# Kernel optimization log

Hardware: AMD Instinct MI355X
Metric: run time of the kernel (lower is better)

## Reference

```python
import jax, jax.numpy as jnp
import numpy as np

N = 200000
M = 100000
K = 27
C = 128
NEG_SLOPE = 0.2


def setup_inputs() -> dict:
    key = jax.random.key(0)
    ks = jax.random.split(key, 7)
    feats = jax.random.normal(ks[0], (N, C), dtype=jnp.float32)
    # small init scale (mirrors xavier * 0.1) to keep activations stable through 27-tap convs
    W1 = jax.random.normal(ks[1], (K, C, C), dtype=jnp.float32) * 0.02
    W2 = jax.random.normal(ks[2], (C, C), dtype=jnp.float32) * 0.05
    W3 = jax.random.normal(ks[3], (K, C, C), dtype=jnp.float32) * 0.02
    in_map = jax.random.randint(ks[4], (K, M), 0, N, dtype=jnp.int32)
    out_map = jax.random.randint(ks[5], (K, M), 0, N, dtype=jnp.int32)
    mask = jax.random.uniform(ks[6], (N, 1), dtype=jnp.float32)
    return {"feats": feats, "W1": W1, "W2": W2, "W3": W3,
            "in_map": in_map, "out_map": out_map, "mask": mask}


def _lrelu(x):
    return jnp.where(x >= 0, x, NEG_SLOPE * x)


def _sparse_conv(feats, W, in_map, out_map, n_out):
    """Gather-GEMM-scatter sparse conv: scan over K kernel offsets.

    feats: [N, Cin]; W: [K, Cin, Cout]; in_map/out_map: [K, M].
    """
    def body(acc, xs):
        im, om, w = xs
        y = feats[im] @ w                    # [M, Cin] @ [Cin, Cout]
        return acc.at[om].add(y), None
    out0 = jnp.zeros((n_out, W.shape[-1]), feats.dtype)
    out, _ = jax.lax.scan(body, out0, (in_map, out_map, W))
    return out


def reference(feats, W1, W2, W3, in_map, out_map, mask):
    n = feats.shape[0]
    c1 = _lrelu(_sparse_conv(feats, W1, in_map, out_map, n))   # conv1 (k=3) + LeakyReLU
    c2 = _lrelu(c1 @ W2)                                       # conv2 (k=1) + LeakyReLU
    c3 = _sparse_conv(c2, W3, in_map, out_map, n)              # conv3 (k=3)
    return c3 * mask
```

## Files before the change

kernel.cpp:

```cpp
#include <hip/hip_runtime.h>
#include <hip/hip_bf16.h>


typedef __attribute__((ext_vector_type(8))) short short8;
typedef __attribute__((ext_vector_type(4))) float f32x4;

#define CDIM 128
#define BM   128
#define NEG_SLOPE 0.2f

__device__ __forceinline__ unsigned short f2bf(float x) {
    union { float f; unsigned u; } un; un.f = x;
    unsigned r = un.u + 0x7fffu + ((un.u >> 16) & 1u);
    return (unsigned short)(r >> 16);
}

__device__ __forceinline__ float lrelu(float x) {
    return x >= 0.f ? x : NEG_SLOPE * x;
}

__device__ __forceinline__ int swz(int r, int c) {
    return (r << 7) + ((((c >> 3) ^ (r & 15)) << 3));
}

__global__ void cvt_feats_kernel(const float* __restrict__ in,
                                 unsigned short* __restrict__ out, int n4) {
    int i = blockIdx.x * blockDim.x + threadIdx.x;
    if (i >= n4) return;
    float4 v = reinterpret_cast<const float4*>(in)[i];
    ushort4 o;
    o.x = f2bf(v.x); o.y = f2bf(v.y); o.z = f2bf(v.z); o.w = f2bf(v.w);
    reinterpret_cast<ushort4*>(out)[i] = o;
}

__global__ void cvt_weights_kernel(const float* __restrict__ W1,
                                   const float* __restrict__ W2,
                                   const float* __restrict__ W3,
                                   unsigned short* __restrict__ W1t,
                                   unsigned short* __restrict__ W2t,
                                   unsigned short* __restrict__ W3t) {
    const int KW = 27 * 128 * 128;
    int t = blockIdx.x * blockDim.x + threadIdx.x;
    if (t < KW) {
        int k = t >> 14, r = t & 16383, n = r >> 7, kk = r & 127;
        W1t[t] = f2bf(W1[(k << 14) + (kk << 7) + n]);
    } else if (t < 2 * KW) {
        int t2 = t - KW;
        int k = t2 >> 14, r = t2 & 16383, n = r >> 7, kk = r & 127;
        W3t[t2] = f2bf(W3[(k << 14) + (kk << 7) + n]);
    } else if (t < 2 * KW + 16384) {
        int t2 = t - 2 * KW;
        int n = t2 >> 7, kk = t2 & 127;
        W2t[t2] = f2bf(W2[(kk << 7) + n]);
    }
}

__global__ __launch_bounds__(256, 2)
void sconv_kernel(const unsigned short* __restrict__ A,
                  const unsigned short* __restrict__ Wt,
                  const int* __restrict__ in_map,
                  const int* __restrict__ out_map,
                  float* __restrict__ out,
                  int M) {
    const int k     = blockIdx.y;
    const int mbase = blockIdx.x * BM;
    const int tid   = threadIdx.x;

    __shared__ unsigned short lA[BM * CDIM];
    __shared__ unsigned short lW[CDIM * CDIM];

    const unsigned short* wk = Wt + (size_t)k * 16384;
    #pragma unroll
    for (int i = 0; i < 8; ++i) {
        int flat = (i * 256 + tid) * 8;
        int row = flat >> 7, col = flat & 127;
        short8 v = *reinterpret_cast<const short8*>(wk + flat);
        *reinterpret_cast<short8*>(&lW[swz(row, col)]) = v;
    }

    const int* imk = in_map + (size_t)k * M;
    #pragma unroll
    for (int p = 0; p < 8; ++p) {
        int r = p * 16 + (tid >> 4);
        int c = (tid & 15) * 8;
        int m = mbase + r;
        short8 v = {0, 0, 0, 0, 0, 0, 0, 0};
        if (m < M) {
            int arow = __ldg(imk + m);
            v = *reinterpret_cast<const short8*>(A + (size_t)arow * CDIM + c);
        }
        *reinterpret_cast<short8*>(&lA[swz(r, c)]) = v;
    }
    __syncthreads();

    const int wid  = tid >> 6, lane = tid & 63;
    const int wr   = (wid >> 1) * 64, wc = (wid & 1) * 64;
    const int lrow = lane & 15, quad = lane >> 4;

    f32x4 acc[4][4];
    #pragma unroll
    for (int i = 0; i < 4; ++i)
        #pragma unroll
        for (int j = 0; j < 4; ++j)
            acc[i][j] = {0.f, 0.f, 0.f, 0.f};

    #pragma unroll
    for (int s = 0; s < 4; ++s) {
        const int kf = s * 32 + quad * 8;
        short8 a[4], b[4];
        #pragma unroll
        for (int i = 0; i < 4; ++i)
            a[i] = *reinterpret_cast<const short8*>(&lA[swz(wr + i * 16 + lrow, kf)]);
        #pragma unroll
        for (int j = 0; j < 4; ++j)
            b[j] = *reinterpret_cast<const short8*>(&lW[swz(wc + j * 16 + lrow, kf)]);
        #pragma unroll
        for (int i = 0; i < 4; ++i)
            #pragma unroll
            for (int j = 0; j < 4; ++j)
                acc[i][j] = __builtin_amdgcn_mfma_f32_16x16x32_bf16(a[i], b[j], acc[i][j], 0, 0, 0);
    }

    const int* omk = out_map + (size_t)k * M;
    #pragma unroll
    for (int i = 0; i < 4; ++i) {
        #pragma unroll
        for (int reg = 0; reg < 4; ++reg) {
            int m = mbase + wr + i * 16 + quad * 4 + reg;
            if (m < M) {
                int orow = __ldg(omk + m);
                float* dst = out + (size_t)orow * CDIM + wc + lrow;
                #pragma unroll
                for (int j = 0; j < 4; ++j)
                    unsafeAtomicAdd(dst + j * 16, acc[i][j][reg]);
            }
        }
    }
}

__global__ __launch_bounds__(256, 2)
void conv2_kernel(const float* __restrict__ c1,
                  const unsigned short* __restrict__ W2t,
                  unsigned short* __restrict__ c2,
                  int M) {
    const int mbase = blockIdx.x * BM;
    const int tid   = threadIdx.x;

    __shared__ unsigned short lA[BM * CDIM];
    __shared__ unsigned short lW[CDIM * CDIM];

    #pragma unroll
    for (int i = 0; i < 8; ++i) {
        int flat = (i * 256 + tid) * 8;
        int row = flat >> 7, col = flat & 127;
        short8 v = *reinterpret_cast<const short8*>(W2t + flat);
        *reinterpret_cast<short8*>(&lW[swz(row, col)]) = v;
    }

    #pragma unroll
    for (int p = 0; p < 8; ++p) {
        int r = p * 16 + (tid >> 4);
        int c = (tid & 15) * 8;
        int m = mbase + r;
        unsigned short vv[8];
        if (m < M) {
            const float4* src = reinterpret_cast<const float4*>(c1 + (size_t)m * CDIM + c);
            float4 x0 = src[0], x1 = src[1];
            vv[0] = f2bf(lrelu(x0.x)); vv[1] = f2bf(lrelu(x0.y));
            vv[2] = f2bf(lrelu(x0.z)); vv[3] = f2bf(lrelu(x0.w));
            vv[4] = f2bf(lrelu(x1.x)); vv[5] = f2bf(lrelu(x1.y));
            vv[6] = f2bf(lrelu(x1.z)); vv[7] = f2bf(lrelu(x1.w));
        } else {
            #pragma unroll
            for (int q = 0; q < 8; ++q) vv[q] = 0;
        }
        short8 v;
        #pragma unroll
        for (int q = 0; q < 8; ++q) v[q] = (short)vv[q];
        *reinterpret_cast<short8*>(&lA[swz(r, c)]) = v;
    }
    __syncthreads();

    const int wid  = tid >> 6, lane = tid & 63;
    const int wr   = (wid >> 1) * 64, wc = (wid & 1) * 64;
    const int lrow = lane & 15, quad = lane >> 4;

    f32x4 acc[4][4];
    #pragma unroll
    for (int i = 0; i < 4; ++i)
        #pragma unroll
        for (int j = 0; j < 4; ++j)
            acc[i][j] = {0.f, 0.f, 0.f, 0.f};

    #pragma unroll
    for (int s = 0; s < 4; ++s) {
        const int kf = s * 32 + quad * 8;
        short8 a[4], b[4];
        #pragma unroll
        for (int i = 0; i < 4; ++i)
            a[i] = *reinterpret_cast<const short8*>(&lA[swz(wr + i * 16 + lrow, kf)]);
        #pragma unroll
        for (int j = 0; j < 4; ++j)
            b[j] = *reinterpret_cast<const short8*>(&lW[swz(wc + j * 16 + lrow, kf)]);
        #pragma unroll
        for (int i = 0; i < 4; ++i)
            #pragma unroll
            for (int j = 0; j < 4; ++j)
                acc[i][j] = __builtin_amdgcn_mfma_f32_16x16x32_bf16(a[i], b[j], acc[i][j], 0, 0, 0);
    }

    #pragma unroll
    for (int i = 0; i < 4; ++i) {
        #pragma unroll
        for (int reg = 0; reg < 4; ++reg) {
            int m = mbase + wr + i * 16 + quad * 4 + reg;
            if (m < M) {
                unsigned short* dst = c2 + (size_t)m * CDIM + wc + lrow;
                #pragma unroll
                for (int j = 0; j < 4; ++j)
                    dst[j * 16] = f2bf(lrelu(acc[i][j][reg]));
            }
        }
    }
}

__global__ void mask_mul_kernel(float* __restrict__ out,
                                const float* __restrict__ mask, int n4) {
    int i = blockIdx.x * blockDim.x + threadIdx.x;
    if (i >= n4) return;
    int row = i >> 5;
    float m = mask[row];
    float4 v = reinterpret_cast<float4*>(out)[i];
    v.x *= m; v.y *= m; v.z *= m; v.w *= m;
    reinterpret_cast<float4*>(out)[i] = v;
}

extern "C" void kernel_launch(void* const* d_in, const int* in_sizes, int n_in,
                              void* d_out, int out_size, void* d_ws, size_t ws_size,
                              hipStream_t stream) {
    const float* feats   = (const float*)d_in[0];
    const float* W1      = (const float*)d_in[1];
    const float* W2      = (const float*)d_in[2];
    const float* W3      = (const float*)d_in[3];
    const int*   in_map  = (const int*)d_in[4];
    const int*   out_map = (const int*)d_in[5];
    const float* mask    = (const float*)d_in[6];
    float*       out     = (float*)d_out;

    const int K = 27;
    const int N = in_sizes[0] / CDIM;
    const int M = in_sizes[4] / K;

    unsigned short* feats_bf = (unsigned short*)d_ws;
    unsigned short* c2_bf    = feats_bf + (size_t)N * CDIM;
    unsigned short* W1t      = c2_bf + (size_t)N * CDIM;
    unsigned short* W3t      = W1t + (size_t)K * CDIM * CDIM;
    unsigned short* W2t      = W3t + (size_t)K * CDIM * CDIM;
    size_t need = ((size_t)2 * N * CDIM + (size_t)2 * K * CDIM * CDIM + CDIM * CDIM) * 2;
    if (ws_size < need) return;

    const int n4 = N * CDIM / 4;
    cvt_feats_kernel<<<(n4 + 255) / 256, 256, 0, stream>>>(feats, feats_bf, n4);
    const int wtot = 2 * K * CDIM * CDIM + CDIM * CDIM;
    cvt_weights_kernel<<<(wtot + 255) / 256, 256, 0, stream>>>(W1, W2, W3, W1t, W2t, W3t);

    hipMemsetAsync(d_out, 0, (size_t)N * CDIM * sizeof(float), stream);

    dim3 gs((M + BM - 1) / BM, K);
    sconv_kernel<<<gs, 256, 0, stream>>>(feats_bf, W1t, in_map, out_map, out, M);

    conv2_kernel<<<(N + BM - 1) / BM, 256, 0, stream>>>(out, W2t, c2_bf, N);

    hipMemsetAsync(d_out, 0, (size_t)N * CDIM * sizeof(float), stream);
    sconv_kernel<<<gs, 256, 0, stream>>>(c2_bf, W3t, in_map, out_map, out, M);

    mask_mul_kernel<<<(n4 + 255) / 256, 256, 0, stream>>>(out, mask, n4);
}
```

Baseline: 2.530 ms.

## Bucket gather-scatter pairs by output tile and accumulate in LDS

Builds a per-output-tile, per-tap bucketing of (in_row, out_row, k) pairs with a histogram, a three-kernel scan and an atomic scatter. Each conv then runs one block per 128-row output tile, accumulating MFMA results into an LDS float tile with shared atomics instead of global atomics. LeakyReLU and bf16 conversion are fused into the conv1 epilogue and the mask multiply into the conv3 epilogue, which removes both output memsets and the standalone mask kernel. The cost is extra preprocessing kernels, weights read straight from global memory for every pair, and load imbalance because the grid is only about 1563 blocks.

```diff
diff --git a/kernel.cpp b/kernel.cpp
--- a/kernel.cpp
+++ b/kernel.cpp
@@ -7,6 +7,7 @@
 
 #define CDIM 128
 #define BM   128
+#define KTAPS 27
 #define NEG_SLOPE 0.2f
 
 __device__ __forceinline__ unsigned short f2bf(float x) {
@@ -39,7 +40,7 @@
                                    unsigned short* __restrict__ W1t,
                                    unsigned short* __restrict__ W2t,
                                    unsigned short* __restrict__ W3t) {
-    const int KW = 27 * 128 * 128;
+    const int KW = KTAPS * 128 * 128;
     int t = blockIdx.x * blockDim.x + threadIdx.x;
     if (t < KW) {
         int k = t >> 14, r = t & 16383, n = r >> 7, kk = r & 127;
@@ -55,40 +56,179 @@
     }
 }
 
+__global__ void hist_kernel(const int* __restrict__ out_map,
+                            int* __restrict__ cnt, int M) {
+    int m = blockIdx.x * 256 + threadIdx.x;
+    if (m >= M) return;
+    int k = blockIdx.y;
+    int orow = out_map[(size_t)k * M + m];
+    atomicAdd(cnt + ((orow >> 7) * KTAPS + k), 1);
+}
+
+__global__ void scan_a_kernel(const int* __restrict__ cnt, int* __restrict__ cs,
+                              int* __restrict__ partials, int NB) {
+    __shared__ int sd[256];
+    int tid = threadIdx.x, bin = blockIdx.x * 256 + tid;
+    int v = (bin < NB) ? ((cnt[bin] + 15) >> 4) : 0;
+    sd[tid] = v; __syncthreads();
+    for (int off = 1; off < 256; off <<= 1) {
+        int t = (tid >= off) ? sd[tid - off] : 0; __syncthreads();
+        sd[tid] += t; __syncthreads();
+    }
+    if (bin < NB) cs[bin] = sd[tid] - v;
+    if (tid == 255) partials[blockIdx.x] = sd[255];
+}
+
+__global__ void scan_b_kernel(int* __restrict__ partials, int NBb) {
+    __shared__ int sd[256];
+    int tid = threadIdx.x;
+    int v = (tid < NBb) ? partials[tid] : 0;
+    sd[tid] = v; __syncthreads();
+    for (int off = 1; off < 256; off <<= 1) {
+        int t = (tid >= off) ? sd[tid - off] : 0; __syncthreads();
+        sd[tid] += t; __syncthreads();
+    }
+    partials[tid] = sd[tid] - v;
+}
+
+__global__ void scan_c_kernel(int* __restrict__ cs, const int* __restrict__ partials,
+                              int NB, int NBb) {
+    int bin = blockIdx.x * 256 + threadIdx.x;
+    if (bin < NB) cs[bin] += partials[blockIdx.x];
+    if (bin == 0) cs[NB] = partials[NBb];
+}
+
+__global__ void fill_kernel(int* __restrict__ p, int n, int v) {
+    int i = blockIdx.x * 256 + threadIdx.x;
+    if (i < n) p[i] = v;
+}
+
+__global__ void scatter_kernel(const int* __restrict__ in_map,
+                               const int* __restrict__ out_map,
+                               const int* __restrict__ cs,
+                               int* __restrict__ cursor,
+                               int* __restrict__ pairs, int M) {
+    int m = blockIdx.x * 256 + threadIdx.x;
+    if (m >= M) return;
+    int k = blockIdx.y;
+    size_t e = (size_t)k * M + m;
+    int orow = out_map[e], irow = in_map[e];
+    int bin = (orow >> 7) * KTAPS + k;
+    int pos = atomicAdd(cursor + bin, 1);
+    pairs[(size_t)cs[bin] * 16 + pos] = (k << 26) | (irow << 8) | (orow & 127);
+}
+
+template<int MODE>
+__global__ __launch_bounds__(512, 4)
+void conv_fused_kernel(const unsigned short* __restrict__ A,
+                       const unsigned short* __restrict__ Wt,
+                       const int* __restrict__ pairs,
+                       const int* __restrict__ cs,
+                       unsigned short* __restrict__ bf_out,
+                       float* __restrict__ f_out,
+                       const float* __restrict__ mask,
+                       int N) {
+    __shared__ float lacc[128 * 128];
+    const int tid  = threadIdx.x;
+    const int tile = blockIdx.x;
+
+    #pragma unroll
+    for (int i = tid; i < 128 * 128 / 4; i += 512)
+        reinterpret_cast<f32x4*>(lacc)[i] = (f32x4){0.f, 0.f, 0.f, 0.f};
+    __syncthreads();
+
+    const int lo = cs[tile * KTAPS], hi = cs[tile * KTAPS + KTAPS];
+    const int wid = tid >> 6, lane = tid & 63;
+    const int lrow = lane & 15, quad = lane >> 4;
+
+    const int total = hi - lo;
+    const int per   = (total + 7) >> 3;
+    const int c0 = lo + wid * per;
+    const int c1 = (c0 + per < hi) ? (c0 + per) : hi;
+
+    for (int c = c0; c < c1; ++c) {
+        int pk   = pairs[c * 16 + lrow];
+        int irow = (pk >> 8) & 0x3FFFF;
+        int srow = pk & 0x7F;
+        int k    = ((unsigned)__shfl(pk, 0)) >> 26;
+
+        const unsigned short* wk = Wt + ((size_t)k << 14);
+        const unsigned short* ar = A + (size_t)irow * CDIM + quad * 8;
+        short8 a0 = *reinterpret_cast<const short8*>(ar);
+        short8 a1 = *reinterpret_cast<const short8*>(ar + 32);
+        short8 a2 = *reinterpret_cast<const short8*>(ar + 64);
+        short8 a3 = *reinterpret_cast<const short8*>(ar + 96);
+
+        int sr0 = __shfl(srow, quad * 4 + 0);
+        int sr1 = __shfl(srow, quad * 4 + 1);
+        int sr2 = __shfl(srow, quad * 4 + 2);
+        int sr3 = __shfl(srow, quad * 4 + 3);
+
+        #pragma unroll 2
+        for (int j = 0; j < 8; ++j) {
+            const unsigned short* wb = wk + ((j * 16 + lrow) << 7) + quad * 8;
+            f32x4 acc = {0.f, 0.f, 0.f, 0.f};
+            acc = __builtin_amdgcn_mfma_f32_16x16x32_bf16(a0, *reinterpret_cast<const short8*>(wb),      acc, 0, 0, 0);
+            acc = __builtin_amdgcn_mfma_f32_16x16x32_bf16(a1, *reinterpret_cast<const short8*>(wb + 32), acc, 0, 0, 0);
+            acc = __builtin_amdgcn_mfma_f32_16x16x32_bf16(a2, *reinterpret_cast<const short8*>(wb + 64), acc, 0, 0, 0);
+            acc = __builtin_amdgcn_mfma_f32_16x16x32_bf16(a3, *reinterpret_cast<const short8*>(wb + 96), acc, 0, 0, 0);
+            float* colp = lacc + j * 16 + lrow;
+            atomicAdd(colp + (sr0 << 7), acc[0]);
+            atomicAdd(colp + (sr1 << 7), acc[1]);
+            atomicAdd(colp + (sr2 << 7), acc[2]);
+            atomicAdd(colp + (sr3 << 7), acc[3]);
+        }
+    }
+    __syncthreads();
+
+    const int gbase = tile << 7;
+    #pragma unroll
+    for (int it = 0; it < 8; ++it) {
+        int flat = it * 512 + tid;
+        int r = flat >> 5, c4 = flat & 31;
+        int g = gbase + r;
+        if (g < N) {
+            f32x4 v = *reinterpret_cast<f32x4*>(&lacc[r * CDIM + c4 * 4]);
+            if (MODE == 0) {
+                ushort4 o;
+                o.x = f2bf(lrelu(v[0])); o.y = f2bf(lrelu(v[1]));
+                o.z = f2bf(lrelu(v[2])); o.w = f2bf(lrelu(v[3]));
+                *reinterpret_cast<ushort4*>(bf_out + (size_t)g * CDIM + c4 * 4) = o;
+            } else {
+                float mv = mask[g];
+                f32x4 o = {v[0] * mv, v[1] * mv, v[2] * mv, v[3] * mv};
+                *reinterpret_cast<f32x4*>(f_out + (size_t)g * CDIM + c4 * 4) = o;
+            }
+        }
+    }
+}
+
 __global__ __launch_bounds__(256, 2)
-void sconv_kernel(const unsigned short* __restrict__ A,
-                  const unsigned short* __restrict__ Wt,
-                  const int* __restrict__ in_map,
-                  const int* __restrict__ out_map,
-                  float* __restrict__ out,
-                  int M) {
-    const int k     = blockIdx.y;
+void conv2_kernel(const unsigned short* __restrict__ c1,
+                  const unsigned short* __restrict__ W2t,
+                  unsigned short* __restrict__ c2,
+                  int N) {
     const int mbase = blockIdx.x * BM;
     const int tid   = threadIdx.x;
 
     __shared__ unsigned short lA[BM * CDIM];
     __shared__ unsigned short lW[CDIM * CDIM];
 
-    const unsigned short* wk = Wt + (size_t)k * 16384;
     #pragma unroll
     for (int i = 0; i < 8; ++i) {
         int flat = (i * 256 + tid) * 8;
         int row = flat >> 7, col = flat & 127;
-        short8 v = *reinterpret_cast<const short8*>(wk + flat);
+        short8 v = *reinterpret_cast<const short8*>(W2t + flat);
         *reinterpret_cast<short8*>(&lW[swz(row, col)]) = v;
     }
 
-    const int* imk = in_map + (size_t)k * M;
     #pragma unroll
     for (int p = 0; p < 8; ++p) {
         int r = p * 16 + (tid >> 4);
         int c = (tid & 15) * 8;
         int m = mbase + r;
         short8 v = {0, 0, 0, 0, 0, 0, 0, 0};
-        if (m < M) {
-            int arow = __ldg(imk + m);
-            v = *reinterpret_cast<const short8*>(A + (size_t)arow * CDIM + c);
-        }
+        if (m < N) v = *reinterpret_cast<const short8*>(c1 + (size_t)m * CDIM + c);
         *reinterpret_cast<short8*>(&lA[swz(r, c)]) = v;
     }
     __syncthreads();
@@ -121,100 +261,12 @@
                 acc[i][j] = __builtin_amdgcn_mfma_f32_16x16x32_bf16(a[i], b[j], acc[i][j], 0, 0, 0);
     }
 
-    const int* omk = out_map + (size_t)k * M;
     #pragma unroll
     for (int i = 0; i < 4; ++i) {
         #pragma unroll
         for (int reg = 0; reg < 4; ++reg) {
             int m = mbase + wr + i * 16 + quad * 4 + reg;
-            if (m < M) {
-                int orow = __ldg(omk + m);
-                float* dst = out + (size_t)orow * CDIM + wc + lrow;
-                #pragma unroll
-                for (int j = 0; j < 4; ++j)
-                    unsafeAtomicAdd(dst + j * 16, acc[i][j][reg]);
-            }
-        }
-    }
-}
-
-__global__ __launch_bounds__(256, 2)
-void conv2_kernel(const float* __restrict__ c1,
-                  const unsigned short* __restrict__ W2t,
-                  unsigned short* __restrict__ c2,
-                  int M) {
-    const int mbase = blockIdx.x * BM;
-    const int tid   = threadIdx.x;
-
-    __shared__ unsigned short lA[BM * CDIM];
-    __shared__ unsigned short lW[CDIM * CDIM];
-
-    #pragma unroll
-    for (int i = 0; i < 8; ++i) {
-        int flat = (i * 256 + tid) * 8;
-        int row = flat >> 7, col = flat & 127;
-        short8 v = *reinterpret_cast<const short8*>(W2t + flat);
-        *reinterpret_cast<short8*>(&lW[swz(row, col)]) = v;
-    }
-
-    #pragma unroll
-    for (int p = 0; p < 8; ++p) {
-        int r = p * 16 + (tid >> 4);
-        int c = (tid & 15) * 8;
-        int m = mbase + r;
-        unsigned short vv[8];
-        if (m < M) {
-            const float4* src = reinterpret_cast<const float4*>(c1 + (size_t)m * CDIM + c);
-            float4 x0 = src[0], x1 = src[1];
-            vv[0] = f2bf(lrelu(x0.x)); vv[1] = f2bf(lrelu(x0.y));
-            vv[2] = f2bf(lrelu(x0.z)); vv[3] = f2bf(lrelu(x0.w));
-            vv[4] = f2bf(lrelu(x1.x)); vv[5] = f2bf(lrelu(x1.y));
-            vv[6] = f2bf(lrelu(x1.z)); vv[7] = f2bf(lrelu(x1.w));
-        } else {
-            #pragma unroll
-            for (int q = 0; q < 8; ++q) vv[q] = 0;
-        }
-        short8 v;
-        #pragma unroll
-        for (int q = 0; q < 8; ++q) v[q] = (short)vv[q];
-        *reinterpret_cast<short8*>(&lA[swz(r, c)]) = v;
-    }
-    __syncthreads();
-
-    const int wid  = tid >> 6, lane = tid & 63;
-    const int wr   = (wid >> 1) * 64, wc = (wid & 1) * 64;
-    const int lrow = lane & 15, quad = lane >> 4;
-
-    f32x4 acc[4][4];
-    #pragma unroll
-    for (int i = 0; i < 4; ++i)
-        #pragma unroll
-        for (int j = 0; j < 4; ++j)
-            acc[i][j] = {0.f, 0.f, 0.f, 0.f};
-
-    #pragma unroll
-    for (int s = 0; s < 4; ++s) {
-        const int kf = s * 32 + quad * 8;
-        short8 a[4], b[4];
-        #pragma unroll
-        for (int i = 0; i < 4; ++i)
-            a[i] = *reinterpret_cast<const short8*>(&lA[swz(wr + i * 16 + lrow, kf)]);
-        #pragma unroll
-        for (int j = 0; j < 4; ++j)
-            b[j] = *reinterpret_cast<const short8*>(&lW[swz(wc + j * 16 + lrow, kf)]);
-        #pragma unroll
-        for (int i = 0; i < 4; ++i)
-            #pragma unroll
-            for (int j = 0; j < 4; ++j)
-                acc[i][j] = __builtin_amdgcn_mfma_f32_16x16x32_bf16(a[i], b[j], acc[i][j], 0, 0, 0);
-    }
-
-    #pragma unroll
-    for (int i = 0; i < 4; ++i) {
-        #pragma unroll
-        for (int reg = 0; reg < 4; ++reg) {
-            int m = mbase + wr + i * 16 + quad * 4 + reg;
-            if (m < M) {
+            if (m < N) {
                 unsigned short* dst = c2 + (size_t)m * CDIM + wc + lrow;
                 #pragma unroll
                 for (int j = 0; j < 4; ++j)
@@ -222,17 +274,6 @@
             }
         }
     }
-}
-
-__global__ void mask_mul_kernel(float* __restrict__ out,
-                                const float* __restrict__ mask, int n4) {
-    int i = blockIdx.x * blockDim.x + threadIdx.x;
-    if (i >= n4) return;
-    int row = i >> 5;
-    float m = mask[row];
-    float4 v = reinterpret_cast<float4*>(out)[i];
-    v.x *= m; v.y *= m; v.z *= m; v.w *= m;
-    reinterpret_cast<float4*>(out)[i] = v;
 }
 
 extern "C" void kernel_launch(void* const* d_in, const int* in_sizes, int n_in,
@@ -247,32 +288,50 @@
     const float* mask    = (const float*)d_in[6];
     float*       out     = (float*)d_out;
 
-    const int K = 27;
-    const int N = in_sizes[0] / CDIM;
-    const int M = in_sizes[4] / K;
-
-    unsigned short* feats_bf = (unsigned short*)d_ws;
-    unsigned short* c2_bf    = feats_bf + (size_t)N * CDIM;
-    unsigned short* W1t      = c2_bf + (size_t)N * CDIM;
-    unsigned short* W3t      = W1t + (size_t)K * CDIM * CDIM;
-    unsigned short* W2t      = W3t + (size_t)K * CDIM * CDIM;
-    size_t need = ((size_t)2 * N * CDIM + (size_t)2 * K * CDIM * CDIM + CDIM * CDIM) * 2;
-    if (ws_size < need) return;
+    const int K   = KTAPS;
+    const int N   = in_sizes[0] / CDIM;
+    const int M   = in_sizes[4] / K;
+    const int NT  = (N + 127) >> 7;
+    const int NB  = NT * K;
+    const int NBb = (NB + 255) >> 8;
+    const int CAP = K * M + 16 * NB;
+
+    char* w = (char*)d_ws;
+    size_t o = 0;
+    auto alloc = [&](size_t bytes) -> void* {
+        void* p = w + o; o = (o + bytes + 511) & ~(size_t)511; return p;
+    };
+    unsigned short* Abf  = (unsigned short*)alloc((size_t)(N + 1) * CDIM * 2);
+    unsigned short* W1t  = (unsigned short*)alloc((size_t)K * CDIM * CDIM * 2);
+    unsigned short* W3t  = (unsigned short*)alloc((size_t)K * CDIM * CDIM * 2);
+    unsigned short* W2t  = (unsigned short*)alloc((size_t)CDIM * CDIM * 2);
+    int* cnt      = (int*)alloc((size_t)NB * 4);
+    int* cursor   = (int*)alloc((size_t)NB * 4);
+    int* cs       = (int*)alloc((size_t)(NB + 1) * 4);
+    int* partials = (int*)alloc(256 * 4);
+    int* pairs    = (int*)alloc((size_t)CAP * 4);
+    if (o > ws_size) return;
+
+    unsigned short* c1bf = (unsigned short*)d_out;
 
     const int n4 = N * CDIM / 4;
-    cvt_feats_kernel<<<(n4 + 255) / 256, 256, 0, stream>>>(feats, feats_bf, n4);
+    cvt_feats_kernel<<<(n4 + 255) / 256, 256, 0, stream>>>(feats, Abf, n4);
+    hipMemsetAsync(Abf + (size_t)N * CDIM, 0, CDIM * 2, stream);
     const int wtot = 2 * K * CDIM * CDIM + CDIM * CDIM;
     cvt_weights_kernel<<<(wtot + 255) / 256, 256, 0, stream>>>(W1, W2, W3, W1t, W2t, W3t);
 
-    hipMemsetAsync(d_out, 0, (size_t)N * CDIM * sizeof(float), stream);
-
-    dim3 gs((M + BM - 1) / BM, K);
-    sconv_kernel<<<gs, 256, 0, stream>>>(feats_bf, W1t, in_map, out_map, out, M);
-
-    conv2_kernel<<<(N + BM - 1) / BM, 256, 0, stream>>>(out, W2t, c2_bf, N);
-
-    hipMemsetAsync(d_out, 0, (size_t)N * CDIM * sizeof(float), stream);
-    sconv_kernel<<<gs, 256, 0, stream>>>(c2_bf, W3t, in_map, out_map, out, M);
-
-    mask_mul_kernel<<<(n4 + 255) / 256, 256, 0, stream>>>(out, mask, n4);
-}
+    hipMemsetAsync(cnt, 0, (size_t)NB * 4, stream);
+    hipMemsetAsync(cursor, 0, (size_t)NB * 4, stream);
+    dim3 gmap((M + 255) / 256, K);
+    hist_kernel<<<gmap, 256, 0, stream>>>(out_map, cnt, M);
+    scan_a_kernel<<<NBb, 256, 0, stream>>>(cnt, cs, partials, NB);
+    scan_b_kernel<<<1, 256, 0, stream>>>(partials, NBb);
+    scan_c_kernel<<<NBb, 256, 0, stream>>>(cs, partials, NB, NBb);
+    const int DUMMY = (N << 8);
+    fill_kernel<<<(CAP + 255) / 256, 256, 0, stream>>>(pairs, CAP, DUMMY);
+    scatter_kernel<<<gmap, 256, 0, stream>>>(in_map, out_map, cs, cursor, pairs, M);
+
+    conv_fused_kernel<0><<<NT, 512, 0, stream>>>(Abf, W1t, pairs, cs, c1bf, nullptr, nullptr, N);
+    conv2_kernel<<<NT, 256, 0, stream>>>(c1bf, W2t, Abf, N);
+    conv_fused_kernel<1><<<NT, 512, 0, stream>>>(Abf, W3t, pairs, cs, nullptr, out, mask, N);
+}
```

Result: slower. 4.916 ms (+94.3%).
